# Kernel tuning notes

Hardware: AMD Instinct MI355X
Metric: run time of the kernel (lower is better)

The kernel has to match this reference:

```python
import jax, jax.numpy as jnp
import numpy as np

N = 50000      # num nodes
E = 800000     # num edges (before self-loops)
DIN = 256
DOUT = 256
K = 3


def setup_inputs() -> dict:
    key = jax.random.key(0)
    k1, k2, k3 = jax.random.split(key, 3)
    x = jax.random.normal(k1, (N, DIN), dtype=jnp.float32)
    edge_index = jax.random.randint(k2, (2, E), 0, N, dtype=jnp.int32)
    # xavier_uniform for weight [K+1, DIN, DOUT]
    limit = float(np.sqrt(6.0 / (DIN + DOUT)))
    weight = jax.random.uniform(k3, (K + 1, DIN, DOUT), dtype=jnp.float32,
                                minval=-limit, maxval=limit)
    bias = jnp.zeros((DOUT,), dtype=jnp.float32)
    return {"x": x, "edge_index": edge_index, "weight": weight, "bias": bias}


def reference(x, edge_index, weight, bias):
    num_nodes = x.shape[0]
    # add self loops
    loops = jnp.arange(num_nodes, dtype=edge_index.dtype)
    row = jnp.concatenate([edge_index[0], loops])
    col = jnp.concatenate([edge_index[1], loops])
    # degree of row (including self loops)
    deg = jax.ops.segment_sum(jnp.ones_like(row, dtype=x.dtype), row,
                              num_segments=num_nodes)
    deg_inv_sqrt = jnp.where(deg > 0, jax.lax.rsqrt(jnp.maximum(deg, 1e-30)), 0.0)
    # edge-weighted Laplacian values: -D^{-1/2} A D^{-1/2}, +1 on diagonal
    Lvals = -deg_inv_sqrt[row] * deg_inv_sqrt[col]
    Lvals = jnp.where(row == col, Lvals + 1.0, Lvals)

    def spmm(v):  # [N, D] -> [N, D]
        return jax.ops.segment_sum(Lvals[:, None] * v[col], row,
                                   num_segments=num_nodes)

    out = jnp.matmul(x, weight[0])
    Tx_0 = x
    Tx_1 = spmm(x)
    out = out + jnp.matmul(Tx_1, weight[1])
    for k in range(2, K + 1):
        Tx_2 = 2.0 * spmm(Tx_1) - Tx_0
        out = out + jnp.matmul(Tx_2, weight[k])
        Tx_0, Tx_1 = Tx_1, Tx_2
    return out + bias
```

## Files before the change

### kernel.cpp

```cpp
#include <hip/hip_runtime.h>
#include <hip/hip_bf16.h>

#define DFEAT 256

typedef __attribute__((ext_vector_type(8))) short bf16x8;
typedef __attribute__((ext_vector_type(4))) float f32x4;

__device__ __forceinline__ float bf2f(unsigned short u) {
  return __builtin_bit_cast(float, ((unsigned)u) << 16);
}
__device__ __forceinline__ unsigned short f2bf(float f) {
  __hip_bfloat16 h = __float2bfloat16(f);
  return *reinterpret_cast<unsigned short*>(&h);
}
__device__ __forceinline__ void gload_lds16(const void* g, void* l) {
  __builtin_amdgcn_global_load_lds(
      (const __attribute__((address_space(1))) void*)g,
      (__attribute__((address_space(3))) void*)l, 16, 0, 0);
}


__global__ void k_count(const int* __restrict__ ei0, int E, int* __restrict__ cnt) {
  int i = blockIdx.x * blockDim.x + threadIdx.x;
  if (i < E) atomicAdd(&cnt[ei0[i]], 1);
}

__global__ __launch_bounds__(256) void k_scan1(const int* __restrict__ cnt, int N,
                                               int* __restrict__ incl,
                                               int* __restrict__ bsum,
                                               float* __restrict__ dis) {
  __shared__ int sh[256];
  int t = threadIdx.x;
  int i = blockIdx.x * 256 + t;
  int v = (i < N) ? cnt[i] : 0;
  sh[t] = v;
  __syncthreads();
  for (int o = 1; o < 256; o <<= 1) {
    int u = (t >= o) ? sh[t - o] : 0;
    __syncthreads();
    sh[t] += u;
    __syncthreads();
  }
  if (i < N) {
    incl[i] = sh[t];
    dis[i] = rsqrtf((float)(v + 1));
  }
  if (t == 255) bsum[blockIdx.x] = sh[255];
}

__global__ __launch_bounds__(256) void k_scan2(const int* __restrict__ bsum, int nb,
                                               int* __restrict__ boff) {
  __shared__ int sh[256];
  int t = threadIdx.x;
  int v = (t < nb) ? bsum[t] : 0;
  sh[t] = v;
  __syncthreads();
  for (int o = 1; o < 256; o <<= 1) {
    int u = (t >= o) ? sh[t - o] : 0;
    __syncthreads();
    sh[t] += u;
    __syncthreads();
  }
  if (t < nb) boff[t] = sh[t] - v;
}

__global__ __launch_bounds__(256) void k_scan3(const int* __restrict__ cnt,
                                               const int* __restrict__ incl,
                                               const int* __restrict__ boff, int N, int E,
                                               int* __restrict__ rowptr) {
  int i = blockIdx.x * 256 + threadIdx.x;
  if (i < N) rowptr[i] = boff[blockIdx.x] + incl[i] - cnt[i];
  if (i == 0) rowptr[N] = E;
}

__global__ void k_scatter(const int* __restrict__ ei0, const int* __restrict__ ei1, int E,
                          const int* __restrict__ rowptr, int* __restrict__ cursor,
                          int* __restrict__ cols) {
  int i = blockIdx.x * blockDim.x + threadIdx.x;
  if (i >= E) return;
  int r = ei0[i];
  int pos = rowptr[r] + atomicAdd(&cursor[r], 1);
  cols[pos] = ei1[i];
}


__global__ void k_f2bf(const float* __restrict__ src, unsigned short* __restrict__ dst,
                       int n4) {
  int i = blockIdx.x * blockDim.x + threadIdx.x;
  if (i >= n4) return;
  float4 f = *(const float4*)(src + (size_t)i * 4);
  ushort4 u;
  u.x = f2bf(f.x); u.y = f2bf(f.y); u.z = f2bf(f.z); u.w = f2bf(f.w);
  *(ushort4*)(dst + (size_t)i * 4) = u;
}

__global__ __launch_bounds__(256) void k_wt(const float* __restrict__ W,
                                            unsigned short* __restrict__ WT) {
  int idx = blockIdx.x * 256 + threadIdx.x;
  int n = idx & 255;
  int k = idx >> 8;
  float w0 = W[idx];
  float w1 = W[65536 + idx];
  float w2 = W[2 * 65536 + idx];
  float w3 = W[3 * 65536 + idx];
  int t = (n << 8) | k;
  WT[t]               = f2bf(w0 - w2);
  WT[65536 + t]       = f2bf(w1 - 3.0f * w3);
  WT[2 * 65536 + t]   = f2bf(2.0f * w2);
  WT[3 * 65536 + t]   = f2bf(4.0f * w3);
}


__global__ __launch_bounds__(256) void k_spmm_bf(
    const unsigned short* __restrict__ v, unsigned short* __restrict__ y,
    const int* __restrict__ rowptr, const int* __restrict__ cols,
    const float* __restrict__ dis) {
  __shared__ float red[3][32][9];
  int r = blockIdx.x;
  int lane = threadIdx.x & 63;
  int w4 = threadIdx.x >> 6;
  int half = lane >> 5;
  int l32 = lane & 31;
  int slot = w4 * 2 + half;
  int fo = l32 * 8;
  float acc[8] = {};
  int e0 = rowptr[r], e1 = rowptr[r + 1];
  float dr = dis[r];

  int e = e0 + slot;
  for (; e + 8 < e1; e += 16) {
    int cA = cols[e], cB = cols[e + 8];
    float lA = -dr * dis[cA] + (cA == r ? 1.f : 0.f);
    float lB = -dr * dis[cB] + (cB == r ? 1.f : 0.f);
    uint4 uA = *(const uint4*)(v + (size_t)cA * DFEAT + fo);
    uint4 uB = *(const uint4*)(v + (size_t)cB * DFEAT + fo);
    const unsigned int* wa = &uA.x;
    const unsigned int* wb = &uB.x;
#pragma unroll
    for (int j = 0; j < 4; ++j) {
      acc[2 * j]     += lA * bf2f(wa[j] & 0xffff) + lB * bf2f(wb[j] & 0xffff);
      acc[2 * j + 1] += lA * bf2f(wa[j] >> 16)    + lB * bf2f(wb[j] >> 16);
    }
  }
  if (e < e1) {
    int c = cols[e];
    float lv = -dr * dis[c] + (c == r ? 1.f : 0.f);
    uint4 u = *(const uint4*)(v + (size_t)c * DFEAT + fo);
    const unsigned int* wu = &u.x;
#pragma unroll
    for (int j = 0; j < 4; ++j) {
      acc[2 * j]     += lv * bf2f(wu[j] & 0xffff);
      acc[2 * j + 1] += lv * bf2f(wu[j] >> 16);
    }
  }

#pragma unroll
  for (int j = 0; j < 8; ++j) acc[j] += __shfl_xor(acc[j], 32);

  if (w4 && !half) {
#pragma unroll
    for (int j = 0; j < 8; ++j) red[w4 - 1][l32][j] = acc[j];
  }
  __syncthreads();
  if (w4 == 0 && !half) {
    float sc = 1.0f - dr * dr;
    uint4 uv = *(const uint4*)(v + (size_t)r * DFEAT + fo);
    const unsigned int* vu = &uv.x;
    ushort4 o[2];
    unsigned short* op = &o[0].x;
#pragma unroll
    for (int j = 0; j < 8; ++j) {
      float a = acc[j] + red[0][l32][j] + red[1][l32][j] + red[2][l32][j];
      float selfv = (j & 1) ? bf2f(vu[j >> 1] >> 16) : bf2f(vu[j >> 1] & 0xffff);
      op[j] = f2bf(a + sc * selfv);
    }
    *(uint4*)(y + (size_t)r * DFEAT + fo) = *(const uint4*)&o[0];
  }
}


__global__ __launch_bounds__(256) void k_gemm4(
    const unsigned short* __restrict__ A0, const unsigned short* __restrict__ A1,
    const unsigned short* __restrict__ A2, const unsigned short* __restrict__ A3,
    const unsigned short* __restrict__ WT,
    const float* __restrict__ bias, float* __restrict__ C, int N) {
  __shared__ __align__(16) unsigned short As[2][128 * 64];
  __shared__ __align__(16) unsigned short Bs[2][128 * 64];
  int tid = threadIdx.x;
  int lane = tid & 63;
  int w = tid >> 6;
  int wm = w >> 1, wn = w & 1;
  int brow = blockIdx.x * 128;
  int bcol = blockIdx.y * 128;

  f32x4 acc[4][4] = {};

  int srow = w * 32 + (lane >> 3);
  int skb = ((lane & 7) ^ (lane >> 3)) << 4;

  auto stage = [&](int buf, int it) {
    int g = it >> 2;
    int k0 = (it & 3) * 64;
    const unsigned short* Asrc = g == 0 ? A0 : g == 1 ? A1 : g == 2 ? A2 : A3;
    const unsigned short* Bsrc = WT + (g << 16);
#pragma unroll
    for (int c = 0; c < 4; ++c) {
      int r = srow + c * 8;
      int grow = brow + r;
      if (grow >= N) grow = N - 1;
      gload_lds16(Asrc + (size_t)grow * DFEAT + k0 + (skb >> 1),
                  (char*)As[buf] + (w * 32 + c * 8) * 128);
      gload_lds16(Bsrc + (size_t)(bcol + r) * DFEAT + k0 + (skb >> 1),
                  (char*)Bs[buf] + (w * 32 + c * 8) * 128);
    }
  };

  stage(0, 0);
  __syncthreads();

  for (int it = 0; it < 16; ++it) {
    int cur = it & 1;
    if (it < 15) stage(cur ^ 1, it + 1);
#pragma unroll
    for (int ks = 0; ks < 2; ++ks) {
      bf16x8 af[4], bfr[4];
#pragma unroll
      for (int i = 0; i < 4; ++i) {
        int row = wm * 64 + i * 16 + (lane & 15);
        int kb = (ks * 64 + ((lane >> 4) << 4)) ^ ((row & 7) << 4);
        af[i] = *(const bf16x8*)((const char*)As[cur] + row * 128 + kb);
      }
#pragma unroll
      for (int j = 0; j < 4; ++j) {
        int row = wn * 64 + j * 16 + (lane & 15);
        int kb = (ks * 64 + ((lane >> 4) << 4)) ^ ((row & 7) << 4);
        bfr[j] = *(const bf16x8*)((const char*)Bs[cur] + row * 128 + kb);
      }
#pragma unroll
      for (int i = 0; i < 4; ++i)
#pragma unroll
        for (int j = 0; j < 4; ++j)
          acc[i][j] = __builtin_amdgcn_mfma_f32_16x16x32_bf16(af[i], bfr[j], acc[i][j], 0, 0, 0);
    }
    if (it < 15) __syncthreads();
  }

#pragma unroll
  for (int i = 0; i < 4; ++i) {
    int rowb = brow + wm * 64 + i * 16 + (lane >> 4) * 4;
#pragma unroll
    for (int j = 0; j < 4; ++j) {
      int col = bcol + wn * 64 + j * 16 + (lane & 15);
      float b = bias[col];
#pragma unroll
      for (int q = 0; q < 4; ++q) {
        int r = rowb + q;
        if (r < N) C[(size_t)r * DFEAT + col] = acc[i][j][q] + b;
      }
    }
  }
}


extern "C" void kernel_launch(void* const* d_in, const int* in_sizes, int n_in,
                              void* d_out, int out_size, void* d_ws, size_t ws_size,
                              hipStream_t stream) {
  const float* x = (const float*)d_in[0];
  const int* ei = (const int*)d_in[1];
  const float* weight = (const float*)d_in[2];
  const float* bias = (const float*)d_in[3];
  float* out = (float*)d_out;

  int N = in_sizes[0] / DFEAT;
  int E = in_sizes[1] / 2;
  const int* ei0 = ei;
  const int* ei1 = ei + E;

  char* ws = (char*)d_ws;
  size_t off = 0;
  auto alloc = [&](size_t bytes) {
    void* p = ws + off;
    off = (off + bytes + 255) & ~(size_t)255;
    return p;
  };
  int* cnt = (int*)alloc((size_t)2 * N * sizeof(int));
  int* cursor = cnt + N;
  int* rowptr = (int*)alloc((size_t)(N + 1) * sizeof(int));
  float* dis = (float*)alloc((size_t)N * sizeof(float));
  int* cols = (int*)alloc((size_t)E * sizeof(int));
  int* incl = (int*)alloc((size_t)N * sizeof(int));
  int* bsum = (int*)alloc(256 * sizeof(int));
  int* boff = (int*)alloc(256 * sizeof(int));
  unsigned short* xbf = (unsigned short*)alloc((size_t)N * DFEAT * 2);
  unsigned short* S1 = (unsigned short*)alloc((size_t)N * DFEAT * 2);
  unsigned short* S2 = (unsigned short*)alloc((size_t)N * DFEAT * 2);
  unsigned short* S3 = (unsigned short*)alloc((size_t)N * DFEAT * 2);
  unsigned short* WT = (unsigned short*)alloc((size_t)4 * DFEAT * DFEAT * 2);

  hipMemsetAsync(cnt, 0, (size_t)2 * N * sizeof(int), stream);

  int eb = (E + 255) / 256;
  int nb = (N + 255) / 256;
  k_count<<<eb, 256, 0, stream>>>(ei0, E, cnt);
  k_scan1<<<nb, 256, 0, stream>>>(cnt, N, incl, bsum, dis);
  k_scan2<<<1, 256, 0, stream>>>(bsum, nb, boff);
  k_scan3<<<nb, 256, 0, stream>>>(cnt, incl, boff, N, E, rowptr);
  k_scatter<<<eb, 256, 0, stream>>>(ei0, ei1, E, rowptr, cursor, cols);

  int n4 = N * DFEAT / 4;
  k_f2bf<<<(n4 + 255) / 256, 256, 0, stream>>>(x, xbf, n4);
  k_wt<<<DFEAT * DFEAT / 256, 256, 0, stream>>>(weight, WT);

  k_spmm_bf<<<N, 256, 0, stream>>>(xbf, S1, rowptr, cols, dis);
  k_spmm_bf<<<N, 256, 0, stream>>>(S1, S2, rowptr, cols, dis);
  k_spmm_bf<<<N, 256, 0, stream>>>(S2, S3, rowptr, cols, dis);

  dim3 ggrid((N + 127) / 128, DFEAT / 128);
  k_gemm4<<<ggrid, 256, 0, stream>>>(xbf, S1, S2, S3, WT, bias, out, N);
}
```

Baseline: 360.8 us.

## Map one wavefront per row in SpMM, removing LDS reduction and block sync

The SpMM kernel now assigns each of four wavefronts in a block its own output row, with each lane covering four features using 8-byte loads. Previously a whole 256-thread block shared one row and combined its partial sums through shuffles, LDS and __syncthreads. The change removes that reduction and barrier overhead and launches a quarter as many blocks. In exchange each wavefront walks its edges serially, two at a time, so there is less memory-level parallelism per row and rows of very different degree can leave waves in a block unevenly loaded.

```diff
diff --git a/kernel.cpp b/kernel.cpp
--- a/kernel.cpp
+++ b/kernel.cpp
@@ -114,68 +114,48 @@
 __global__ __launch_bounds__(256) void k_spmm_bf(
     const unsigned short* __restrict__ v, unsigned short* __restrict__ y,
     const int* __restrict__ rowptr, const int* __restrict__ cols,
-    const float* __restrict__ dis) {
-  __shared__ float red[3][32][9];
-  int r = blockIdx.x;
+    const float* __restrict__ dis, int N) {
+  int r = blockIdx.x * 4 + (threadIdx.x >> 6);
+  if (r >= N) return;
   int lane = threadIdx.x & 63;
-  int w4 = threadIdx.x >> 6;
-  int half = lane >> 5;
-  int l32 = lane & 31;
-  int slot = w4 * 2 + half;
-  int fo = l32 * 8;
-  float acc[8] = {};
+  int fo = lane * 4;
   int e0 = rowptr[r], e1 = rowptr[r + 1];
   float dr = dis[r];
-
-  int e = e0 + slot;
-  for (; e + 8 < e1; e += 16) {
-    int cA = cols[e], cB = cols[e + 8];
+  float a0 = 0.f, a1 = 0.f, a2 = 0.f, a3 = 0.f;
+
+  int e = e0;
+  for (; e + 1 < e1; e += 2) {
+    int cA = cols[e], cB = cols[e + 1];
     float lA = -dr * dis[cA] + (cA == r ? 1.f : 0.f);
     float lB = -dr * dis[cB] + (cB == r ? 1.f : 0.f);
-    uint4 uA = *(const uint4*)(v + (size_t)cA * DFEAT + fo);
-    uint4 uB = *(const uint4*)(v + (size_t)cB * DFEAT + fo);
-    const unsigned int* wa = &uA.x;
-    const unsigned int* wb = &uB.x;
-#pragma unroll
-    for (int j = 0; j < 4; ++j) {
-      acc[2 * j]     += lA * bf2f(wa[j] & 0xffff) + lB * bf2f(wb[j] & 0xffff);
-      acc[2 * j + 1] += lA * bf2f(wa[j] >> 16)    + lB * bf2f(wb[j] >> 16);
-    }
+    uint2 uA = *(const uint2*)(v + (size_t)cA * DFEAT + fo);
+    uint2 uB = *(const uint2*)(v + (size_t)cB * DFEAT + fo);
+    a0 += lA * bf2f(uA.x & 0xffff) + lB * bf2f(uB.x & 0xffff);
+    a1 += lA * bf2f(uA.x >> 16)    + lB * bf2f(uB.x >> 16);
+    a2 += lA * bf2f(uA.y & 0xffff) + lB * bf2f(uB.y & 0xffff);
+    a3 += lA * bf2f(uA.y >> 16)    + lB * bf2f(uB.y >> 16);
   }
   if (e < e1) {
     int c = cols[e];
     float lv = -dr * dis[c] + (c == r ? 1.f : 0.f);
-    uint4 u = *(const uint4*)(v + (size_t)c * DFEAT + fo);
-    const unsigned int* wu = &u.x;
-#pragma unroll
-    for (int j = 0; j < 4; ++j) {
-      acc[2 * j]     += lv * bf2f(wu[j] & 0xffff);
-      acc[2 * j + 1] += lv * bf2f(wu[j] >> 16);
-    }
-  }
-
-#pragma unroll
-  for (int j = 0; j < 8; ++j) acc[j] += __shfl_xor(acc[j], 32);
-
-  if (w4 && !half) {
-#pragma unroll
-    for (int j = 0; j < 8; ++j) red[w4 - 1][l32][j] = acc[j];
-  }
-  __syncthreads();
-  if (w4 == 0 && !half) {
-    float sc = 1.0f - dr * dr;
-    uint4 uv = *(const uint4*)(v + (size_t)r * DFEAT + fo);
-    const unsigned int* vu = &uv.x;
-    ushort4 o[2];
-    unsigned short* op = &o[0].x;
-#pragma unroll
-    for (int j = 0; j < 8; ++j) {
-      float a = acc[j] + red[0][l32][j] + red[1][l32][j] + red[2][l32][j];
-      float selfv = (j & 1) ? bf2f(vu[j >> 1] >> 16) : bf2f(vu[j >> 1] & 0xffff);
-      op[j] = f2bf(a + sc * selfv);
-    }
-    *(uint4*)(y + (size_t)r * DFEAT + fo) = *(const uint4*)&o[0];
-  }
+    uint2 u = *(const uint2*)(v + (size_t)c * DFEAT + fo);
+    a0 += lv * bf2f(u.x & 0xffff);
+    a1 += lv * bf2f(u.x >> 16);
+    a2 += lv * bf2f(u.y & 0xffff);
+    a3 += lv * bf2f(u.y >> 16);
+  }
+
+  float sc = 1.0f - dr * dr;
+  uint2 uv = *(const uint2*)(v + (size_t)r * DFEAT + fo);
+  a0 += sc * bf2f(uv.x & 0xffff);
+  a1 += sc * bf2f(uv.x >> 16);
+  a2 += sc * bf2f(uv.y & 0xffff);
+  a3 += sc * bf2f(uv.y >> 16);
+
+  uint2 o;
+  o.x = (unsigned)f2bf(a0) | ((unsigned)f2bf(a1) << 16);
+  o.y = (unsigned)f2bf(a2) | ((unsigned)f2bf(a3) << 16);
+  *(uint2*)(y + (size_t)r * DFEAT + fo) = o;
 }
 
 
@@ -311,9 +291,10 @@
   k_f2bf<<<(n4 + 255) / 256, 256, 0, stream>>>(x, xbf, n4);
   k_wt<<<DFEAT * DFEAT / 256, 256, 0, stream>>>(weight, WT);
 
-  k_spmm_bf<<<N, 256, 0, stream>>>(xbf, S1, rowptr, cols, dis);
-  k_spmm_bf<<<N, 256, 0, stream>>>(S1, S2, rowptr, cols, dis);
-  k_spmm_bf<<<N, 256, 0, stream>>>(S2, S3, rowptr, cols, dis);
+  int sgrid = (N + 3) / 4;
+  k_spmm_bf<<<sgrid, 256, 0, stream>>>(xbf, S1, rowptr, cols, dis, N);
+  k_spmm_bf<<<sgrid, 256, 0, stream>>>(S1, S2, rowptr, cols, dis, N);
+  k_spmm_bf<<<sgrid, 256, 0, stream>>>(S2, S3, rowptr, cols, dis, N);
 
   dim3 ggrid((N + 127) / 128, DFEAT / 128);
   k_gemm4<<<ggrid, 256, 0, stream>>>(xbf, S1, S2, S3, WT, bias, out, N);
```

New measurement: 369.2 us. +2.3%, slower.
